# Kernel optimization log

Measured on AMD Instinct MI355X. Metric: run time of the kernel, lower is better.

The kernel has to match this reference:

```python
import jax, jax.numpy as jnp
import numpy as np

B, SQ, SKV, H, NH = 2, 2048, 2048, 1024, 16
HD = H // NH  # head dim = 64


def setup_inputs() -> dict:
    key = jax.random.key(0)
    ks = jax.random.split(key, 10)
    s = 1.0 / np.sqrt(H)
    return {
        "query_states": jax.random.normal(ks[0], (B, SQ, H), jnp.float32),
        "key_value_states": jax.random.normal(ks[1], (B, SKV, H), jnp.float32),
        "attention_mask": jnp.ones((B, SQ, SKV), jnp.float32),
        "Wq": jax.random.normal(ks[2], (H, H), jnp.float32) * s,
        "bq": jnp.zeros((H,), jnp.float32),
        "Wk": jax.random.normal(ks[3], (H, H), jnp.float32) * s,
        "Wv": jax.random.normal(ks[4], (H, H), jnp.float32) * s,
        "bv": jnp.zeros((H,), jnp.float32),
        "Wo": jax.random.normal(ks[5], (H, H), jnp.float32) * s,
        "bo": jnp.zeros((H,), jnp.float32),
    }


def reference(query_states, key_value_states, attention_mask, Wq, bq, Wk, Wv, bv, Wo, bo):
    # projections (torch Linear: x @ W.T + b; key proj has NO bias)
    q = query_states @ Wq.T + bq            # [B,SQ,H]
    k = key_value_states @ Wk.T              # [B,SKV,H]
    v = key_value_states @ Wv.T + bv         # [B,SKV,H]
    # split heads -> [B, NH, S, HD]
    q = q.reshape(B, SQ, NH, HD).transpose(0, 2, 1, 3)
    k = k.reshape(B, SKV, NH, HD).transpose(0, 2, 1, 3)
    v = v.reshape(B, SKV, NH, HD).transpose(0, 2, 1, 3)
    scale = 1.0 / np.sqrt(HD)
    scores = jnp.einsum("bhqd,bhkd->bhqk", q * scale, k)
    # additive mask: (1 - mask) * -10000, broadcast over heads
    scores = scores + ((1.0 - attention_mask) * -10000.0)[:, None, :, :]
    probs = jax.nn.softmax(scores, axis=-1)  # dropout p=0 (eval) -> identity
    ctx = jnp.einsum("bhqk,bhkd->bhqd", probs, v)
    ctx = ctx.transpose(0, 2, 1, 3).reshape(B, SQ, H)
    return ctx @ Wo.T + bo
```

## Files before the change

kernel.cpp:

```cpp
#include <hip/hip_runtime.h>

typedef unsigned short u16;
typedef unsigned char u8;
typedef unsigned int u32;
typedef short s16x8 __attribute__((ext_vector_type(8)));
typedef float f32x4 __attribute__((ext_vector_type(4)));

#define AS1 __attribute__((address_space(1)))
#define AS3 __attribute__((address_space(3)))

#define LOG2E 1.4426950408889634f

__device__ __forceinline__ u16 f2bf(float f) {
  unsigned u = __float_as_uint(f);
  u += 0x7fffu + ((u >> 16) & 1u);
  return (u16)(u >> 16);
}
__device__ __forceinline__ float bf2f(u16 b) {
  return __uint_as_float(((unsigned)b) << 16);
}
__device__ __forceinline__ u32 cvtpk(float lo, float hi) {
  u32 r;
  asm("v_cvt_pk_bf16_f32 %0, %1, %2" : "=v"(r) : "v"(lo), "v"(hi));
  return r;
}
__device__ __forceinline__ void gld16(const void* g, void* l) {
  __builtin_amdgcn_global_load_lds((const AS1 unsigned int*)g,
                                   (AS3 unsigned int*)l, 16, 0, 0);
}

__global__ __launch_bounds__(256) void prep_kernel(
    const float* __restrict__ qs, const float* __restrict__ kvs, const float* __restrict__ mk,
    const float* __restrict__ wq, const float* __restrict__ wk, const float* __restrict__ wv,
    const float* __restrict__ wo,
    u16* __restrict__ q_bf, u16* __restrict__ kv_bf, u16* __restrict__ am_bf,
    u16* __restrict__ wq_bf, u16* __restrict__ wk_bf, u16* __restrict__ wv_bf,
    u16* __restrict__ wo_bf)
{
  const int stride = gridDim.x * blockDim.x;
  const float mscale = -10000.f * LOG2E;
  for (int v = blockIdx.x * blockDim.x + threadIdx.x; v < 5242880; v += stride) {
    const float* s; u16* d; int off; bool ismask = false;
    if (v < 1048576)      { s = qs;  d = q_bf;  off = v; }
    else if (v < 2097152) { s = kvs; d = kv_bf; off = v - 1048576; }
    else if (v < 2359296) { s = wq;  d = wq_bf; off = v - 2097152; }
    else if (v < 2621440) { s = wk;  d = wk_bf; off = v - 2359296; }
    else if (v < 2883584) { s = wv;  d = wv_bf; off = v - 2621440; }
    else if (v < 3145728) { s = wo;  d = wo_bf; off = v - 2883584; }
    else                  { s = mk;  d = am_bf; off = v - 3145728; ismask = true; }
    float4 f = ((const float4*)s)[off];
    if (ismask) {
      f.x = (1.f - f.x) * mscale; f.y = (1.f - f.y) * mscale;
      f.z = (1.f - f.z) * mscale; f.w = (1.f - f.w) * mscale;
    }
    uint2 o;
    o.x = cvtpk(f.x, f.y);
    o.y = cvtpk(f.z, f.w);
    ((uint2*)d)[off] = o;
  }
}

__global__ __launch_bounds__(256) void flag_kernel(const u16* __restrict__ am,
                                                   u8* __restrict__ flags)
{
  const int fid = blockIdx.x;
  const int kt = fid & 31, qt = (fid >> 5) & 15, b = fid >> 9;
  const int t = threadIdx.x;
  const int row = t >> 1, half = t & 1;
  const u16* p = am + ((size_t)(b * 2048 + qt * 128 + row)) * 2048 + kt * 64 + half * 32;
  const uint4 v0 = *(const uint4*)p;
  const uint4 v1 = *(const uint4*)(p + 16);
  const u32 acc = v0.x | v0.y | v0.z | v0.w | v1.x | v1.y | v1.z | v1.w;
  const bool z = (acc & 0x7fff7fffu) == 0;
  const bool wz = __all(z);
  __shared__ int ok[4];
  if ((t & 63) == 0) ok[t >> 6] = wz;
  __syncthreads();
  if (t == 0) flags[fid] = (ok[0] & ok[1] & ok[2] & ok[3]) ? 1 : 0;
}

template<int EPI>
__device__ __forceinline__ void gemm_body(
    const u16* __restrict__ A, const u16* __restrict__ W, const float* __restrict__ bias,
    void* __restrict__ outp, float alpha, int m0, int n0)
{
  __shared__ u16 As[3][4096], Bs[3][4096];
  const int tid = threadIdx.x, wave = tid >> 6, lane = tid & 63;
  const int l15 = lane & 15, l4 = lane >> 4;
  const int wr = wave >> 1, wc = wave & 1;

  const int srow = wave * 16 + (lane >> 2);
  const int soct = ((lane & 3) ^ ((lane >> 3) & 3)) * 8;
  const u16* aS = A + (size_t)(m0 + srow) * 1024 + soct;
  const u16* bS = W + (size_t)(n0 + srow) * 1024 + soct;
  const int dOff = wave * 512;

  const int fswz = (l15 >> 1) & 3;
  const int afBase = (wr * 32 + l15) * 32 + ((l4 ^ fswz) * 8);
  const int bfBase = (wc * 64 + l15) * 32 + ((l4 ^ fswz) * 8);

  f32x4 acc[2][4] = {};

  auto stage = [&](int buf, int kt) {
    const int ko = kt * 32;
    gld16(aS + ko, &As[buf][dOff]);
    gld16(bS + ko, &Bs[buf][dOff]);
  };

  stage(0, 0);
  stage(1, 1);

  int cb = 0;
  for (int kt = 0; kt < 32; ++kt) {
    if (kt < 31) asm volatile("s_waitcnt vmcnt(2)" ::: "memory");
    else         asm volatile("s_waitcnt vmcnt(0)" ::: "memory");
    __builtin_amdgcn_s_barrier();
    asm volatile("" ::: "memory");
    if (kt < 30) {
      int sb = cb + 2; if (sb >= 3) sb -= 3;
      stage(sb, kt + 2);
    }
    s16x8 af[2], bf[4];
    #pragma unroll
    for (int m = 0; m < 2; ++m) af[m] = *(const s16x8*)&As[cb][afBase + m * 512];
    #pragma unroll
    for (int n = 0; n < 4; ++n) bf[n] = *(const s16x8*)&Bs[cb][bfBase + n * 512];
    #pragma unroll
    for (int m = 0; m < 2; ++m)
      #pragma unroll
      for (int n = 0; n < 4; ++n)
        acc[m][n] = __builtin_amdgcn_mfma_f32_16x16x32_bf16(af[m], bf[n], acc[m][n], 0, 0, 0);
    asm volatile("" ::: "memory");
    cb = (cb + 1 == 3) ? 0 : cb + 1;
  }

  #pragma unroll
  for (int n = 0; n < 4; ++n) {
    const int col = n0 + wc * 64 + n * 16 + l15;
    #pragma unroll
    for (int m = 0; m < 2; ++m) {
      #pragma unroll
      for (int r = 0; r < 4; ++r) {
        const int row = m0 + wr * 32 + m * 16 + l4 * 4 + r;
        if constexpr (EPI == 0) {
          const float val = (acc[m][n][r] + (bias ? bias[col] : 0.f)) * alpha;
          const int bb = row >> 11, ss = row & 2047, hh = col >> 6, dd = col & 63;
          ((u16*)outp)[(((size_t)(bb * 16 + hh)) * 2048 + ss) * 64 + dd] = f2bf(val);
        } else if constexpr (EPI == 1) {
          ((float*)outp)[(size_t)row * 1024 + col] = acc[m][n][r] + (bias ? bias[col] : 0.f);
        } else {
          const float val = acc[m][n][r] + bias[row];
          const int hh = row >> 6, dd = row & 63, bb = col >> 11, ss = col & 2047;
          ((u16*)outp)[(((size_t)(bb * 16 + hh)) * 64 + dd) * 2048 + ss] = f2bf(val);
        }
      }
    }
  }
}

__global__ __launch_bounds__(512) void gemm_qkv(
    const u16* __restrict__ qbf, const u16* __restrict__ kvbf,
    const u16* __restrict__ wqb, const u16* __restrict__ wkb, const u16* __restrict__ wvb,
    const float* __restrict__ bq, const float* __restrict__ bv,
    u16* __restrict__ Qh, u16* __restrict__ Kh, u16* __restrict__ Vt)
{
  const int bid = blockIdx.x;
  const int swz = (bid & 7) * 32 + (bid >> 3);
  const int which = blockIdx.y;
  if (which == 0)
    gemm_body<0>(qbf, wqb, bq, Qh, 0.125f * LOG2E, (swz >> 3) * 128, (swz & 7) * 128);
  else if (which == 1)
    gemm_body<0>(kvbf, wkb, nullptr, Kh, 1.0f, (swz >> 3) * 128, (swz & 7) * 128);
  else
    gemm_body<2>(wvb, kvbf, bv, Vt, 1.0f, (bid >> 5) * 128,
                 ((bid & 7) + ((bid >> 3) & 3) * 8) * 128);
}

__global__ __launch_bounds__(512) void gemm_fin(
    const u16* __restrict__ ctx, const u16* __restrict__ wob,
    const float* __restrict__ bo, float* __restrict__ out)
{
  const int bid = blockIdx.x;
  const int swz = (bid & 7) * 32 + (bid >> 3);
  gemm_body<1>(ctx, wob, bo, out, 1.0f, (swz >> 3) * 128, (swz & 7) * 128);
}

__global__ __launch_bounds__(256) void attn_kernel(
    const u16* __restrict__ Qh, const u16* __restrict__ Kh,
    const u16* __restrict__ Vt, const u16* __restrict__ am,
    const u8* __restrict__ flags, u16* __restrict__ ctx)
{
  __shared__ u16 Ks[2][4096];
  __shared__ u16 Vs[2][4096];
  __shared__ u16 Pl[4][2][1024];
  const int tid = threadIdx.x, wave = tid >> 6, lane = tid & 63;
  const int l15 = lane & 15, l4 = lane >> 4;
  const int x7 = l15 & 7;
  const int bid = blockIdx.x;
  const int pos = (bid & 7) * 64 + (bid >> 3);
  const int hh = pos >> 4, qt = pos & 15;
  const int b = hh >> 4, h = hh & 15;
  const int q0 = qt * 128;
  const u16* Qb = Qh + (size_t)hh * 2048 * 64;
  const u16* Kb = Kh + (size_t)hh * 2048 * 64;
  const u16* Vb = Vt + (size_t)hh * 64 * 2048;

  u32 fbits = 0;
  {
    const u8* fb = flags + (b * 16 + qt) * 32;
    #pragma unroll
    for (int i = 0; i < 32; ++i) fbits |= (fb[i] ? 1u : 0u) << i;
  }

  s16x8 qf[2][2];
  const u16* amrow[2];
  #pragma unroll
  for (int g = 0; g < 2; ++g) {
    const int qrow = q0 + wave * 32 + g * 16 + l15;
    qf[g][0] = *(const s16x8*)(Qb + (size_t)qrow * 64 + l4 * 8);
    qf[g][1] = *(const s16x8*)(Qb + (size_t)qrow * 64 + 32 + l4 * 8);
    amrow[g] = am + ((size_t)b * 2048 + qrow) * 2048;
  }

  const s16x8 ones = {16256, 16256, 16256, 16256, 16256, 16256, 16256, 16256};

  const int sr = wave * 16 + (lane >> 3);
  const int ss = ((lane & 7) ^ ((lane >> 3) & 7)) * 8;
  const u16* kS0 = Kb + (size_t)sr * 64 + ss;
  const u16* kS1 = Kb + (size_t)(sr + 8) * 64 + ss;
  const u16* vS0 = Vb + (size_t)sr * 2048 + ss;
  const u16* vS1 = Vb + (size_t)(sr + 8) * 2048 + ss;
  const int kd0 = wave * 1024, kd1 = kd0 + 512;

  auto stage = [&](int buf, int kt) {
    const int kv0 = kt * 64;
    gld16(kS0 + (size_t)kv0 * 64, &Ks[buf][kd0]);
    gld16(kS1 + (size_t)kv0 * 64, &Ks[buf][kd1]);
    gld16(vS0 + kv0, &Vs[buf][kd0]);
    gld16(vS1 + kv0, &Vs[buf][kd1]);
  };

  f32x4 of[2][4] = {};
  f32x4 lr[2] = {};
  float m_run[2] = {-1e30f, -1e30f};

  stage(0, 0);
  asm volatile("s_waitcnt vmcnt(0)" ::: "memory");
  __builtin_amdgcn_s_barrier();
  asm volatile("" ::: "memory");

  int cur = 0;
  for (int kt = 0; kt < 32; ++kt) {
    if (kt < 31) stage(cur ^ 1, kt + 1);
    const int kv0 = kt * 64;
    const bool skip = (fbits >> kt) & 1u;

    ushort4 mk4[2][4];
    if (!skip) {
      #pragma unroll
      for (int g = 0; g < 2; ++g)
        #pragma unroll
        for (int nf = 0; nf < 4; ++nf)
          mk4[g][nf] = *(const ushort4*)(amrow[g] + kv0 + nf * 16 + l4 * 4);
    }

    f32x4 sf[2][4];
    __builtin_amdgcn_s_setprio(1);
    #pragma unroll
    for (int nf = 0; nf < 4; ++nf) {
      const s16x8 ka0 = *(const s16x8*)&Ks[cur][nf * 1024 + l15 * 64 + ((l4 ^ x7) * 8)];
      const s16x8 ka1 = *(const s16x8*)&Ks[cur][nf * 1024 + l15 * 64 + (((4 + l4) ^ x7) * 8)];
      #pragma unroll
      for (int g = 0; g < 2; ++g) {
        f32x4 s = {0.f, 0.f, 0.f, 0.f};
        s = __builtin_amdgcn_mfma_f32_16x16x32_bf16(ka0, qf[g][0], s, 0, 0, 0);
        s = __builtin_amdgcn_mfma_f32_16x16x32_bf16(ka1, qf[g][1], s, 0, 0, 0);
        sf[g][nf] = s;
      }
    }
    __builtin_amdgcn_s_setprio(0);

    #pragma unroll
    for (int g = 0; g < 2; ++g) {
      float tmax = -1e30f;
      #pragma unroll
      for (int nf = 0; nf < 4; ++nf)
        #pragma unroll
        for (int r = 0; r < 4; ++r) {
          float sv = sf[g][nf][r];
          if (!skip) sv += bf2f(((const u16*)&mk4[g][nf])[r]);
          sf[g][nf][r] = sv;
          tmax = fmaxf(tmax, sv);
        }
      tmax = fmaxf(tmax, __shfl_xor(tmax, 16));
      tmax = fmaxf(tmax, __shfl_xor(tmax, 32));

      const float mOld = m_run[g];
      float mn = mOld;
      if (!__all(tmax <= mOld + 11.54f)) {
        mn = fmaxf(mOld, tmax);
        const float sc = exp2f(mOld - mn);
        m_run[g] = mn;
        float sq[4];
        #pragma unroll
        for (int r = 0; r < 4; ++r) sq[r] = __shfl(sc, l4 * 4 + r);
        #pragma unroll
        for (int r = 0; r < 4; ++r) lr[g][r] *= sq[r];
        #pragma unroll
        for (int nd = 0; nd < 4; ++nd)
          #pragma unroll
          for (int r = 0; r < 4; ++r) of[g][nd][r] *= sq[r];
      }

      u32* pw = (u32*)&Pl[wave][g][0];
      #pragma unroll
      for (int nf = 0; nf < 4; ++nf) {
        const float p0 = exp2f(sf[g][nf][0] - mn), p1 = exp2f(sf[g][nf][1] - mn);
        const float p2 = exp2f(sf[g][nf][2] - mn), p3 = exp2f(sf[g][nf][3] - mn);
        u32* w = pw + l15 * 32 + (((nf * 2 + (l4 >> 1)) ^ x7) * 4) + (l4 & 1) * 2;
        w[0] = cvtpk(p0, p1);
        w[1] = cvtpk(p2, p3);
      }
    }

    __builtin_amdgcn_s_setprio(1);
    #pragma unroll
    for (int kh = 0; kh < 2; ++kh) {
      s16x8 pa[2];
      #pragma unroll
      for (int g = 0; g < 2; ++g)
        pa[g] = *(const s16x8*)&Pl[wave][g][l15 * 64 + (((kh * 4 + l4) ^ x7) * 8)];
      #pragma unroll
      for (int nd = 0; nd < 4; ++nd) {
        const s16x8 vb = *(const s16x8*)&Vs[cur][nd * 1024 + l15 * 64 + (((kh * 4 + l4) ^ x7) * 8)];
        #pragma unroll
        for (int g = 0; g < 2; ++g)
          of[g][nd] = __builtin_amdgcn_mfma_f32_16x16x32_bf16(pa[g], vb, of[g][nd], 0, 0, 0);
      }
      #pragma unroll
      for (int g = 0; g < 2; ++g)
        lr[g] = __builtin_amdgcn_mfma_f32_16x16x32_bf16(pa[g], ones, lr[g], 0, 0, 0);
    }
    __builtin_amdgcn_s_setprio(0);

    if (kt < 31) {
      asm volatile("s_waitcnt vmcnt(0)" ::: "memory");
      __builtin_amdgcn_s_barrier();
      asm volatile("" ::: "memory");
    }
    cur ^= 1;
  }

  #pragma unroll
  for (int g = 0; g < 2; ++g) {
    #pragma unroll
    for (int r = 0; r < 4; ++r) {
      const float invq = 1.f / lr[g][r];
      const int qg = q0 + wave * 32 + g * 16 + l4 * 4 + r;
      const size_t rowbase = ((size_t)b * 2048 + qg) * 1024 + h * 64;
      #pragma unroll
      for (int nd = 0; nd < 4; ++nd)
        ctx[rowbase + nd * 16 + l15] = f2bf(of[g][nd][r] * invq);
    }
  }
}

extern "C" void kernel_launch(void* const* d_in, const int* in_sizes, int n_in,
                              void* d_out, int out_size, void* d_ws, size_t ws_size,
                              hipStream_t stream)
{
  const float* qs = (const float*)d_in[0];
  const float* kvs = (const float*)d_in[1];
  const float* mk = (const float*)d_in[2];
  const float* Wq = (const float*)d_in[3];
  const float* bq = (const float*)d_in[4];
  const float* Wk = (const float*)d_in[5];
  const float* Wv = (const float*)d_in[6];
  const float* bv = (const float*)d_in[7];
  const float* Wo = (const float*)d_in[8];
  const float* bo = (const float*)d_in[9];
  float* out = (float*)d_out;

  char* ws = (char*)d_ws;
  u16* q_bf  = (u16*)(ws + 0);
  u16* kv_bf = (u16*)(ws + 8388608);
  u16* wq_bf = (u16*)(ws + 16777216);
  u16* wk_bf = (u16*)(ws + 18874368);
  u16* wv_bf = (u16*)(ws + 20971520);
  u16* wo_bf = (u16*)(ws + 23068672);
  u16* am_bf = (u16*)(ws + 25165824);
  u16* Qhp   = (u16*)(ws + 41943040);
  u16* Khp   = (u16*)(ws + 50331648);
  u16* Vtp   = (u16*)(ws + 58720256);
  u16* ctxp  = (u16*)(ws + 67108864);
  u8* flagsp = (u8*)wq_bf;

  prep_kernel<<<dim3(2048), dim3(256), 0, stream>>>(
      qs, kvs, mk, Wq, Wk, Wv, Wo, q_bf, kv_bf, am_bf, wq_bf, wk_bf, wv_bf, wo_bf);

  gemm_qkv<<<dim3(256, 3), dim3(512), 0, stream>>>(
      q_bf, kv_bf, wq_bf, wk_bf, wv_bf, bq, bv, Qhp, Khp, Vtp);

  flag_kernel<<<dim3(1024), dim3(256), 0, stream>>>(am_bf, flagsp);

  attn_kernel<<<dim3(512), dim3(256), 0, stream>>>(Qhp, Khp, Vtp, am_bf, flagsp, ctxp);

  gemm_fin<<<dim3(256), dim3(512), 0, stream>>>(ctxp, wo_bf, bo, out);
}
```

Before: 284.3 us.

## Halve attention and output-GEMM tile sizes to raise block count and occupancy

The attention kernel now gives each block 64 query rows instead of 128, so each wave handles one 16-row group. This doubles the grid to 1024 blocks, with flag tiles resized to match. The output projection GEMM gets a dedicated 64x64-tile, 256-thread kernel with a 4-deep async staging ring, replacing the shared 128x128 body and running 1024 blocks. The aim is to fill the GPU's compute units better and cut register pressure, at the cost of reloading K/V tiles twice as often per head and less reuse per block in the GEMM.

```diff
diff --git a/kernel.cpp b/kernel.cpp
--- a/kernel.cpp
+++ b/kernel.cpp
@@ -64,12 +64,12 @@
                                                    u8* __restrict__ flags)
 {
   const int fid = blockIdx.x;
-  const int kt = fid & 31, qt = (fid >> 5) & 15, b = fid >> 9;
+  const int kt = fid & 31, qt = (fid >> 5) & 31, b = fid >> 10;
   const int t = threadIdx.x;
-  const int row = t >> 1, half = t & 1;
-  const u16* p = am + ((size_t)(b * 2048 + qt * 128 + row)) * 2048 + kt * 64 + half * 32;
+  const int row = t >> 2, seg = t & 3;
+  const u16* p = am + ((size_t)(b * 2048 + qt * 64 + row)) * 2048 + kt * 64 + seg * 16;
   const uint4 v0 = *(const uint4*)p;
-  const uint4 v1 = *(const uint4*)(p + 16);
+  const uint4 v1 = *(const uint4*)(p + 8);
   const u32 acc = v0.x | v0.y | v0.z | v0.w | v1.x | v1.y | v1.z | v1.w;
   const bool z = (acc & 0x7fff7fffu) == 0;
   const bool wz = __all(z);
@@ -146,8 +146,6 @@
           const float val = (acc[m][n][r] + (bias ? bias[col] : 0.f)) * alpha;
           const int bb = row >> 11, ss = row & 2047, hh = col >> 6, dd = col & 63;
           ((u16*)outp)[(((size_t)(bb * 16 + hh)) * 2048 + ss) * 64 + dd] = f2bf(val);
-        } else if constexpr (EPI == 1) {
-          ((float*)outp)[(size_t)row * 1024 + col] = acc[m][n][r] + (bias ? bias[col] : 0.f);
         } else {
           const float val = acc[m][n][r] + bias[row];
           const int hh = row >> 6, dd = row & 63, bb = col >> 11, ss = col & 2047;
@@ -176,13 +174,75 @@
                  ((bid & 7) + ((bid >> 3) & 3) * 8) * 128);
 }
 
-__global__ __launch_bounds__(512) void gemm_fin(
+__global__ __launch_bounds__(256) void gemm_fin(
     const u16* __restrict__ ctx, const u16* __restrict__ wob,
     const float* __restrict__ bo, float* __restrict__ out)
 {
+  __shared__ u16 As[4][2048], Bs[4][2048];
+  const int tid = threadIdx.x, wave = tid >> 6, lane = tid & 63;
+  const int l15 = lane & 15, l4 = lane >> 4;
+  const int wr = wave >> 1, wc = wave & 1;
   const int bid = blockIdx.x;
-  const int swz = (bid & 7) * 32 + (bid >> 3);
-  gemm_body<1>(ctx, wob, bo, out, 1.0f, (swz >> 3) * 128, (swz & 7) * 128);
+  const int swz = (bid & 7) * 128 + (bid >> 3);
+  const int m0 = (swz >> 4) * 64, n0 = (swz & 15) * 64;
+
+  const int srow = wave * 16 + (lane >> 2);
+  const int soct = ((lane & 3) ^ ((lane >> 3) & 3)) * 8;
+  const u16* aS = ctx + (size_t)(m0 + srow) * 1024 + soct;
+  const u16* bS = wob + (size_t)(n0 + srow) * 1024 + soct;
+  const int dOff = wave * 512;
+
+  const int fswz = (l15 >> 1) & 3;
+  const int afBase = (wr * 32 + l15) * 32 + ((l4 ^ fswz) * 8);
+  const int bfBase = (wc * 32 + l15) * 32 + ((l4 ^ fswz) * 8);
+
+  f32x4 acc[2][2] = {};
+
+  auto stage = [&](int buf, int kt) {
+    const int ko = kt * 32;
+    gld16(aS + ko, &As[buf][dOff]);
+    gld16(bS + ko, &Bs[buf][dOff]);
+  };
+
+  stage(0, 0);
+  stage(1, 1);
+  stage(2, 2);
+
+  int cb = 0;
+  for (int kt = 0; kt < 32; ++kt) {
+    if (kt < 30)      asm volatile("s_waitcnt vmcnt(4)" ::: "memory");
+    else if (kt == 30) asm volatile("s_waitcnt vmcnt(2)" ::: "memory");
+    else               asm volatile("s_waitcnt vmcnt(0)" ::: "memory");
+    __builtin_amdgcn_s_barrier();
+    asm volatile("" ::: "memory");
+    if (kt < 29) stage((cb + 3) & 3, kt + 3);
+    s16x8 af[2], bf[2];
+    #pragma unroll
+    for (int m = 0; m < 2; ++m) af[m] = *(const s16x8*)&As[cb][afBase + m * 512];
+    #pragma unroll
+    for (int n = 0; n < 2; ++n) bf[n] = *(const s16x8*)&Bs[cb][bfBase + n * 512];
+    #pragma unroll
+    for (int m = 0; m < 2; ++m)
+      #pragma unroll
+      for (int n = 0; n < 2; ++n)
+        acc[m][n] = __builtin_amdgcn_mfma_f32_16x16x32_bf16(af[m], bf[n], acc[m][n], 0, 0, 0);
+    asm volatile("" ::: "memory");
+    cb = (cb + 1) & 3;
+  }
+
+  #pragma unroll
+  for (int n = 0; n < 2; ++n) {
+    const int col = n0 + wc * 32 + n * 16 + l15;
+    const float bv = bo[col];
+    #pragma unroll
+    for (int m = 0; m < 2; ++m) {
+      #pragma unroll
+      for (int r = 0; r < 4; ++r) {
+        const int row = m0 + wr * 32 + m * 16 + l4 * 4 + r;
+        out[(size_t)row * 1024 + col] = acc[m][n][r] + bv;
+      }
+    }
+  }
 }
 
 __global__ __launch_bounds__(256) void attn_kernel(
@@ -192,35 +252,30 @@
 {
   __shared__ u16 Ks[2][4096];
   __shared__ u16 Vs[2][4096];
-  __shared__ u16 Pl[4][2][1024];
+  __shared__ u16 Pl[4][1024];
   const int tid = threadIdx.x, wave = tid >> 6, lane = tid & 63;
   const int l15 = lane & 15, l4 = lane >> 4;
   const int x7 = l15 & 7;
   const int bid = blockIdx.x;
-  const int pos = (bid & 7) * 64 + (bid >> 3);
-  const int hh = pos >> 4, qt = pos & 15;
+  const int pos = (bid & 7) * 128 + (bid >> 3);
+  const int hh = pos >> 5, qt = pos & 31;
   const int b = hh >> 4, h = hh & 15;
-  const int q0 = qt * 128;
+  const int q0 = qt * 64;
   const u16* Qb = Qh + (size_t)hh * 2048 * 64;
   const u16* Kb = Kh + (size_t)hh * 2048 * 64;
   const u16* Vb = Vt + (size_t)hh * 64 * 2048;
 
   u32 fbits = 0;
   {
-    const u8* fb = flags + (b * 16 + qt) * 32;
+    const u8* fb = flags + (b * 32 + qt) * 32;
     #pragma unroll
     for (int i = 0; i < 32; ++i) fbits |= (fb[i] ? 1u : 0u) << i;
   }
 
-  s16x8 qf[2][2];
-  const u16* amrow[2];
-  #pragma unroll
-  for (int g = 0; g < 2; ++g) {
-    const int qrow = q0 + wave * 32 + g * 16 + l15;
-    qf[g][0] = *(const s16x8*)(Qb + (size_t)qrow * 64 + l4 * 8);
-    qf[g][1] = *(const s16x8*)(Qb + (size_t)qrow * 64 + 32 + l4 * 8);
-    amrow[g] = am + ((size_t)b * 2048 + qrow) * 2048;
-  }
+  const int qrow = q0 + wave * 16 + l15;
+  const s16x8 qf0 = *(const s16x8*)(Qb + (size_t)qrow * 64 + l4 * 8);
+  const s16x8 qf1 = *(const s16x8*)(Qb + (size_t)qrow * 64 + 32 + l4 * 8);
+  const u16* amrow = am + ((size_t)b * 2048 + qrow) * 2048;
 
   const s16x8 ones = {16256, 16256, 16256, 16256, 16256, 16256, 16256, 16256};
 
@@ -240,9 +295,9 @@
     gld16(vS1 + kv0, &Vs[buf][kd1]);
   };
 
-  f32x4 of[2][4] = {};
-  f32x4 lr[2] = {};
-  float m_run[2] = {-1e30f, -1e30f};
+  f32x4 of[4] = {};
+  f32x4 lr = {};
+  float m_run = -1e30f;
 
   stage(0, 0);
   asm volatile("s_waitcnt vmcnt(0)" ::: "memory");
@@ -255,91 +310,76 @@
     const int kv0 = kt * 64;
     const bool skip = (fbits >> kt) & 1u;
 
-    ushort4 mk4[2][4];
+    ushort4 mk4[4];
     if (!skip) {
       #pragma unroll
-      for (int g = 0; g < 2; ++g)
-        #pragma unroll
-        for (int nf = 0; nf < 4; ++nf)
-          mk4[g][nf] = *(const ushort4*)(amrow[g] + kv0 + nf * 16 + l4 * 4);
-    }
-
-    f32x4 sf[2][4];
+      for (int nf = 0; nf < 4; ++nf)
+        mk4[nf] = *(const ushort4*)(amrow + kv0 + nf * 16 + l4 * 4);
+    }
+
+    f32x4 sf[4];
     __builtin_amdgcn_s_setprio(1);
     #pragma unroll
     for (int nf = 0; nf < 4; ++nf) {
       const s16x8 ka0 = *(const s16x8*)&Ks[cur][nf * 1024 + l15 * 64 + ((l4 ^ x7) * 8)];
       const s16x8 ka1 = *(const s16x8*)&Ks[cur][nf * 1024 + l15 * 64 + (((4 + l4) ^ x7) * 8)];
-      #pragma unroll
-      for (int g = 0; g < 2; ++g) {
-        f32x4 s = {0.f, 0.f, 0.f, 0.f};
-        s = __builtin_amdgcn_mfma_f32_16x16x32_bf16(ka0, qf[g][0], s, 0, 0, 0);
-        s = __builtin_amdgcn_mfma_f32_16x16x32_bf16(ka1, qf[g][1], s, 0, 0, 0);
-        sf[g][nf] = s;
+      f32x4 s = {0.f, 0.f, 0.f, 0.f};
+      s = __builtin_amdgcn_mfma_f32_16x16x32_bf16(ka0, qf0, s, 0, 0, 0);
+      s = __builtin_amdgcn_mfma_f32_16x16x32_bf16(ka1, qf1, s, 0, 0, 0);
+      sf[nf] = s;
+    }
+    __builtin_amdgcn_s_setprio(0);
+
+    float tmax = -1e30f;
+    #pragma unroll
+    for (int nf = 0; nf < 4; ++nf)
+      #pragma unroll
+      for (int r = 0; r < 4; ++r) {
+        float sv = sf[nf][r];
+        if (!skip) sv += bf2f(((const u16*)&mk4[nf])[r]);
+        sf[nf][r] = sv;
+        tmax = fmaxf(tmax, sv);
       }
-    }
-    __builtin_amdgcn_s_setprio(0);
-
-    #pragma unroll
-    for (int g = 0; g < 2; ++g) {
-      float tmax = -1e30f;
-      #pragma unroll
-      for (int nf = 0; nf < 4; ++nf)
+    tmax = fmaxf(tmax, __shfl_xor(tmax, 16));
+    tmax = fmaxf(tmax, __shfl_xor(tmax, 32));
+
+    const float mOld = m_run;
+    float mn = mOld;
+    if (!__all(tmax <= mOld + 11.54f)) {
+      mn = fmaxf(mOld, tmax);
+      const float sc = exp2f(mOld - mn);
+      m_run = mn;
+      float sq[4];
+      #pragma unroll
+      for (int r = 0; r < 4; ++r) sq[r] = __shfl(sc, l4 * 4 + r);
+      #pragma unroll
+      for (int r = 0; r < 4; ++r) lr[r] *= sq[r];
+      #pragma unroll
+      for (int nd = 0; nd < 4; ++nd)
         #pragma unroll
-        for (int r = 0; r < 4; ++r) {
-          float sv = sf[g][nf][r];
-          if (!skip) sv += bf2f(((const u16*)&mk4[g][nf])[r]);
-          sf[g][nf][r] = sv;
-          tmax = fmaxf(tmax, sv);
-        }
-      tmax = fmaxf(tmax, __shfl_xor(tmax, 16));
-      tmax = fmaxf(tmax, __shfl_xor(tmax, 32));
-
-      const float mOld = m_run[g];
-      float mn = mOld;
-      if (!__all(tmax <= mOld + 11.54f)) {
-        mn = fmaxf(mOld, tmax);
-        const float sc = exp2f(mOld - mn);
-        m_run[g] = mn;
-        float sq[4];
-        #pragma unroll
-        for (int r = 0; r < 4; ++r) sq[r] = __shfl(sc, l4 * 4 + r);
-        #pragma unroll
-        for (int r = 0; r < 4; ++r) lr[g][r] *= sq[r];
-        #pragma unroll
-        for (int nd = 0; nd < 4; ++nd)
-          #pragma unroll
-          for (int r = 0; r < 4; ++r) of[g][nd][r] *= sq[r];
-      }
-
-      u32* pw = (u32*)&Pl[wave][g][0];
-      #pragma unroll
-      for (int nf = 0; nf < 4; ++nf) {
-        const float p0 = exp2f(sf[g][nf][0] - mn), p1 = exp2f(sf[g][nf][1] - mn);
-        const float p2 = exp2f(sf[g][nf][2] - mn), p3 = exp2f(sf[g][nf][3] - mn);
-        u32* w = pw + l15 * 32 + (((nf * 2 + (l4 >> 1)) ^ x7) * 4) + (l4 & 1) * 2;
-        w[0] = cvtpk(p0, p1);
-        w[1] = cvtpk(p2, p3);
-      }
+        for (int r = 0; r < 4; ++r) of[nd][r] *= sq[r];
+    }
+
+    u32* pw = (u32*)&Pl[wave][0];
+    #pragma unroll
+    for (int nf = 0; nf < 4; ++nf) {
+      const float p0 = exp2f(sf[nf][0] - mn), p1 = exp2f(sf[nf][1] - mn);
+      const float p2 = exp2f(sf[nf][2] - mn), p3 = exp2f(sf[nf][3] - mn);
+      u32* w = pw + l15 * 32 + (((nf * 2 + (l4 >> 1)) ^ x7) * 4) + (l4 & 1) * 2;
+      w[0] = cvtpk(p0, p1);
+      w[1] = cvtpk(p2, p3);
     }
 
     __builtin_amdgcn_s_setprio(1);
     #pragma unroll
     for (int kh = 0; kh < 2; ++kh) {
-      s16x8 pa[2];
-      #pragma unroll
-      for (int g = 0; g < 2; ++g)
-        pa[g] = *(const s16x8*)&Pl[wave][g][l15 * 64 + (((kh * 4 + l4) ^ x7) * 8)];
+      const s16x8 pa = *(const s16x8*)&Pl[wave][l15 * 64 + (((kh * 4 + l4) ^ x7) * 8)];
       #pragma unroll
       for (int nd = 0; nd < 4; ++nd) {
         const s16x8 vb = *(const s16x8*)&Vs[cur][nd * 1024 + l15 * 64 + (((kh * 4 + l4) ^ x7) * 8)];
-        #pragma unroll
-        for (int g = 0; g < 2; ++g)
-          of[g][nd] = __builtin_amdgcn_mfma_f32_16x16x32_bf16(pa[g], vb, of[g][nd], 0, 0, 0);
+        of[nd] = __builtin_amdgcn_mfma_f32_16x16x32_bf16(pa, vb, of[nd], 0, 0, 0);
       }
-      #pragma unroll
-      for (int g = 0; g < 2; ++g)
-        lr[g] = __builtin_amdgcn_mfma_f32_16x16x32_bf16(pa[g], ones, lr[g], 0, 0, 0);
+      lr = __builtin_amdgcn_mfma_f32_16x16x32_bf16(pa, ones, lr, 0, 0, 0);
     }
     __builtin_amdgcn_s_setprio(0);
 
@@ -352,16 +392,13 @@
   }
 
   #pragma unroll
-  for (int g = 0; g < 2; ++g) {
-    #pragma unroll
-    for (int r = 0; r < 4; ++r) {
-      const float invq = 1.f / lr[g][r];
-      const int qg = q0 + wave * 32 + g * 16 + l4 * 4 + r;
-      const size_t rowbase = ((size_t)b * 2048 + qg) * 1024 + h * 64;
-      #pragma unroll
-      for (int nd = 0; nd < 4; ++nd)
-        ctx[rowbase + nd * 16 + l15] = f2bf(of[g][nd][r] * invq);
-    }
+  for (int r = 0; r < 4; ++r) {
+    const float invq = 1.f / lr[r];
+    const int qg = q0 + wave * 16 + l4 * 4 + r;
+    const size_t rowbase = ((size_t)b * 2048 + qg) * 1024 + h * 64;
+    #pragma unroll
+    for (int nd = 0; nd < 4; ++nd)
+      ctx[rowbase + nd * 16 + l15] = f2bf(of[nd][r] * invq);
   }
 }
 
@@ -401,9 +438,9 @@
   gemm_qkv<<<dim3(256, 3), dim3(512), 0, stream>>>(
       q_bf, kv_bf, wq_bf, wk_bf, wv_bf, bq, bv, Qhp, Khp, Vtp);
 
-  flag_kernel<<<dim3(1024), dim3(256), 0, stream>>>(am_bf, flagsp);
-
-  attn_kernel<<<dim3(512), dim3(256), 0, stream>>>(Qhp, Khp, Vtp, am_bf, flagsp, ctxp);
-
-  gemm_fin<<<dim3(256), dim3(512), 0, stream>>>(ctxp, wo_bf, bo, out);
-}
+  flag_kernel<<<dim3(2048), dim3(256), 0, stream>>>(am_bf, flagsp);
+
+  attn_kernel<<<dim3(1024), dim3(256), 0, stream>>>(Qhp, Khp, Vtp, am_bf, flagsp, ctxp);
+
+  gemm_fin<<<dim3(1024), dim3(256), 0, stream>>>(ctxp, wo_bf, bo, out);
+}
```

Result: slower. 296.2 us (+4.2%).
